# Kernel optimization log

Hardware: AMD Instinct MI355X
Metric: run time of the kernel (lower is better)

Reference implementation:

```python
import jax, jax.numpy as jnp
import numpy as np

T, B, I, H = 512, 64, 1024, 1024


def setup_inputs() -> dict:
    key = jax.random.key(0)
    ks = jax.random.split(key, 16)
    s_i = 1.0 / np.sqrt(I)  # mimic nn.Linear init scale
    s_h = 1.0 / np.sqrt(H)
    inp = {
        "x": jax.random.normal(ks[0], (T, B, I), dtype=jnp.float32),
        "hidden": jax.random.normal(ks[1], (B, H), dtype=jnp.float32),
        # update gate
        "Wzi": jax.random.normal(ks[2], (H, I), dtype=jnp.float32) * s_i,
        "bzi": jax.random.normal(ks[3], (H,), dtype=jnp.float32) * s_i,
        "Wzh": jax.random.normal(ks[4], (H, H), dtype=jnp.float32) * s_h,
        "bzh": jax.random.normal(ks[5], (H,), dtype=jnp.float32) * s_h,
        # reset gate
        "Wri": jax.random.normal(ks[6], (H, I), dtype=jnp.float32) * s_i,
        "bri": jax.random.normal(ks[7], (H,), dtype=jnp.float32) * s_i,
        "Wrh": jax.random.normal(ks[8], (H, H), dtype=jnp.float32) * s_h,
        "brh": jax.random.normal(ks[9], (H,), dtype=jnp.float32) * s_h,
        # candidate hidden
        "Wci": jax.random.normal(ks[10], (H, I), dtype=jnp.float32) * s_i,
        "bci": jax.random.normal(ks[11], (H,), dtype=jnp.float32) * s_i,
        "Wch": jax.random.normal(ks[12], (H, H), dtype=jnp.float32) * s_h,
        "bch": jax.random.normal(ks[13], (H,), dtype=jnp.float32) * s_h,
    }
    return inp


def reference(x, hidden, Wzi, bzi, Wzh, bzh, Wri, bri, Wrh, brh, Wci, bci, Wch, bch):
    # Pre-compute all input-to-hidden projections in one batched GEMM per gate:
    # [T,B,I] @ [I,H] -> [T,B,H]. Same math as per-step Linear calls.
    xz = jnp.einsum('tbi,hi->tbh', x, Wzi) + bzi
    xr = jnp.einsum('tbi,hi->tbh', x, Wri) + bri
    xc = jnp.einsum('tbi,hi->tbh', x, Wci) + bci

    def step(h, xt):
        xz_t, xr_t, xc_t = xt
        z = jax.nn.sigmoid(xz_t + h @ Wzh.T + bzh)
        r = jax.nn.sigmoid(xr_t + h @ Wrh.T + brh)
        candh = jnp.tanh(xc_t + (r * h) @ Wch.T + bch)
        h_new = (1.0 - z) * h + z * candh
        return h_new, h_new

    hidden_final, output = jax.lax.scan(step, hidden, (xz, xr, xc))
    return output, hidden_final


if __name__ == "__main__":
    out = reference(**setup_inputs())
    print(out[0].shape, out[1].shape)
```

## Files before the change

### kernel.cpp

```cpp
#include <hip/hip_runtime.h>


typedef __bf16 bf16x8 __attribute__((ext_vector_type(8)));
typedef float  f32x4  __attribute__((ext_vector_type(4)));

#define TT 512
#define BB 64
#define HH 1024

__global__ __launch_bounds__(256) void cvt_w(const float* __restrict__ src,
                                             __bf16* __restrict__ dst) {
    int i = (blockIdx.x * 256 + threadIdx.x) * 4;
    f32x4 v = *(const f32x4*)(src + i);
    __bf16 o[4] = {(__bf16)v.x, (__bf16)v.y, (__bf16)v.z, (__bf16)v.w};
    *(ulong1*)(dst + i) = *(ulong1*)o;
}

__global__ __launch_bounds__(256) void gru_init(const float* __restrict__ hid,
                                                float* __restrict__ h_f,
                                                __bf16* __restrict__ h_b) {
    int i = blockIdx.x * 256 + threadIdx.x;
    if (i < BB * HH) {
        float v = hid[i];
        h_f[i] = v;
        h_b[i] = (__bf16)v;
    }
}

__device__ __forceinline__ bf16x8 ld_cvt8(const float* p) {
    f32x4 a = *(const f32x4*)p;
    f32x4 b = *(const f32x4*)(p + 4);
    bf16x8 r;
    r[0] = (__bf16)a.x; r[1] = (__bf16)a.y; r[2] = (__bf16)a.z; r[3] = (__bf16)a.w;
    r[4] = (__bf16)b.x; r[5] = (__bf16)b.y; r[6] = (__bf16)b.z; r[7] = (__bf16)b.w;
    return r;
}

__global__ __launch_bounds__(64) void gru_zr(
    const float* __restrict__ x_t, const __bf16* __restrict__ h_b,
    const float* __restrict__ h_f,
    const __bf16* __restrict__ Wzh, const __bf16* __restrict__ Wzi,
    const float* __restrict__ bzh, const float* __restrict__ bzi,
    const __bf16* __restrict__ Wrh, const __bf16* __restrict__ Wri,
    const float* __restrict__ brh, const float* __restrict__ bri,
    float* __restrict__ zbuf, __bf16* __restrict__ rh)
{
    const int gate_r = blockIdx.x >> 8;
    const int tile   = blockIdx.x & 255;
    const int m0 = (tile & 3) << 4;
    const int n0 = (tile >> 2) << 4;
    const int lane = threadIdx.x;
    const int rc = lane & 15;
    const int kg = lane >> 4;

    const __bf16* Wh = gate_r ? Wrh : Wzh;
    const __bf16* Wi = gate_r ? Wri : Wzi;

    const __bf16* A1 = h_b + (m0 + rc) * HH + kg * 8;
    const __bf16* B1 = Wh  + (n0 + rc) * HH + kg * 8;
    const float*  A2 = x_t + (m0 + rc) * HH + kg * 8;
    const __bf16* B2 = Wi  + (n0 + rc) * HH + kg * 8;

    f32x4 acc = {0.f, 0.f, 0.f, 0.f};
    #pragma unroll 8
    for (int k = 0; k < HH; k += 32) {
        bf16x8 a = *(const bf16x8*)(A1 + k);
        bf16x8 b = *(const bf16x8*)(B1 + k);
        acc = __builtin_amdgcn_mfma_f32_16x16x32_bf16(a, b, acc, 0, 0, 0);
    }
    #pragma unroll 8
    for (int k = 0; k < HH; k += 32) {
        bf16x8 a = ld_cvt8(A2 + k);
        bf16x8 b = *(const bf16x8*)(B2 + k);
        acc = __builtin_amdgcn_mfma_f32_16x16x32_bf16(a, b, acc, 0, 0, 0);
    }

    const int n = n0 + rc;
    const float bias = gate_r ? (brh[n] + bri[n]) : (bzh[n] + bzi[n]);
    #pragma unroll
    for (int r = 0; r < 4; ++r) {
        const int m = m0 + kg * 4 + r;
        const int idx = m * HH + n;
        const float v = acc[r] + bias;
        const float s = 1.f / (1.f + __expf(-v));
        if (gate_r) rh[idx]   = (__bf16)(s * h_f[idx]);
        else        zbuf[idx] = s;
    }
}

__global__ __launch_bounds__(64) void gru_c(
    const float* __restrict__ x_t, const __bf16* __restrict__ rh,
    const __bf16* __restrict__ Wch, const __bf16* __restrict__ Wci,
    const float* __restrict__ bch, const float* __restrict__ bci,
    const float* __restrict__ zbuf,
    float* __restrict__ h_f, __bf16* __restrict__ h_b,
    float* __restrict__ out_t, float* __restrict__ out_tail, int last)
{
    const int tile = blockIdx.x;
    const int m0 = (tile & 3) << 4;
    const int n0 = (tile >> 2) << 4;
    const int lane = threadIdx.x;
    const int rc = lane & 15;
    const int kg = lane >> 4;

    const __bf16* A1 = rh  + (m0 + rc) * HH + kg * 8;
    const __bf16* B1 = Wch + (n0 + rc) * HH + kg * 8;
    const float*  A2 = x_t + (m0 + rc) * HH + kg * 8;
    const __bf16* B2 = Wci + (n0 + rc) * HH + kg * 8;

    f32x4 acc = {0.f, 0.f, 0.f, 0.f};
    #pragma unroll 8
    for (int k = 0; k < HH; k += 32) {
        bf16x8 a = *(const bf16x8*)(A1 + k);
        bf16x8 b = *(const bf16x8*)(B1 + k);
        acc = __builtin_amdgcn_mfma_f32_16x16x32_bf16(a, b, acc, 0, 0, 0);
    }
    #pragma unroll 8
    for (int k = 0; k < HH; k += 32) {
        bf16x8 a = ld_cvt8(A2 + k);
        bf16x8 b = *(const bf16x8*)(B2 + k);
        acc = __builtin_amdgcn_mfma_f32_16x16x32_bf16(a, b, acc, 0, 0, 0);
    }

    const int n = n0 + rc;
    const float bias = bch[n] + bci[n];
    #pragma unroll
    for (int r = 0; r < 4; ++r) {
        const int m = m0 + kg * 4 + r;
        const int idx = m * HH + n;
        const float c = tanhf(acc[r] + bias);
        const float z = zbuf[idx];
        const float hn = (1.f - z) * h_f[idx] + z * c;
        h_f[idx] = hn;
        h_b[idx] = (__bf16)hn;
        out_t[idx] = hn;
        if (last) out_tail[idx] = hn;
    }
}

extern "C" void kernel_launch(void* const* d_in, const int* in_sizes, int n_in,
                              void* d_out, int out_size, void* d_ws, size_t ws_size,
                              hipStream_t stream) {
    const float* x   = (const float*)d_in[0];
    const float* hid = (const float*)d_in[1];
    const float* Wzi = (const float*)d_in[2];
    const float* bzi = (const float*)d_in[3];
    const float* Wzh = (const float*)d_in[4];
    const float* bzh = (const float*)d_in[5];
    const float* Wri = (const float*)d_in[6];
    const float* bri = (const float*)d_in[7];
    const float* Wrh = (const float*)d_in[8];
    const float* brh = (const float*)d_in[9];
    const float* Wci = (const float*)d_in[10];
    const float* bci = (const float*)d_in[11];
    const float* Wch = (const float*)d_in[12];
    const float* bch = (const float*)d_in[13];
    float* out = (float*)d_out;

    char* ws = (char*)d_ws;
    const size_t WSZ = (size_t)HH * HH * sizeof(__bf16);
    __bf16* Wzh_b = (__bf16*)(ws + 0 * WSZ);
    __bf16* Wzi_b = (__bf16*)(ws + 1 * WSZ);
    __bf16* Wrh_b = (__bf16*)(ws + 2 * WSZ);
    __bf16* Wri_b = (__bf16*)(ws + 3 * WSZ);
    __bf16* Wch_b = (__bf16*)(ws + 4 * WSZ);
    __bf16* Wci_b = (__bf16*)(ws + 5 * WSZ);
    char* p = ws + 6 * WSZ;
    float*  zbuf = (float*)p;             p += (size_t)BB * HH * 4;
    float*  h_f  = (float*)p;             p += (size_t)BB * HH * 4;
    __bf16* h_b  = (__bf16*)p;            p += (size_t)BB * HH * 2;
    __bf16* rh   = (__bf16*)p;

    const int cvt_blocks = (HH * HH) / (256 * 4);
    cvt_w<<<cvt_blocks, 256, 0, stream>>>(Wzh, Wzh_b);
    cvt_w<<<cvt_blocks, 256, 0, stream>>>(Wzi, Wzi_b);
    cvt_w<<<cvt_blocks, 256, 0, stream>>>(Wrh, Wrh_b);
    cvt_w<<<cvt_blocks, 256, 0, stream>>>(Wri, Wri_b);
    cvt_w<<<cvt_blocks, 256, 0, stream>>>(Wch, Wch_b);
    cvt_w<<<cvt_blocks, 256, 0, stream>>>(Wci, Wci_b);
    gru_init<<<256, 256, 0, stream>>>(hid, h_f, h_b);

    for (int t = 0; t < TT; ++t) {
        const float* x_t = x + (size_t)t * BB * HH;
        gru_zr<<<512, 64, 0, stream>>>(x_t, h_b, h_f,
                                       Wzh_b, Wzi_b, bzh, bzi,
                                       Wrh_b, Wri_b, brh, bri,
                                       zbuf, rh);
        gru_c<<<256, 64, 0, stream>>>(x_t, rh, Wch_b, Wci_b, bch, bci,
                                      zbuf, h_f, h_b,
                                      out + (size_t)t * BB * HH,
                                      out + (size_t)TT * BB * HH,
                                      (t == TT - 1) ? 1 : 0);
    }
}
```

Baseline: 12.83 ms.

## Fuse GRU timesteps into one persistent kernel with grid-wide barriers

Replaces the 1024 per-step kernel launches with a single persistent kernel of 64 workgroups that loops over all timesteps and synchronises through atomic global barriers. Each workgroup owns a 16-column slice of the hidden units, keeps z in registers and the bf16 x_t tile in LDS, and splits the candidate GEMM's K dimension across wave pairs, combining the halves through LDS. The input projections for the next step are computed while waiting at the barrier, hiding them behind the recurrence. The cost is that only 64 CUs do the work, and progress depends on all workgroups being co-resident and on the spin barrier, which adds latency at each step.

```diff
diff --git a/kernel.cpp b/kernel.cpp
--- a/kernel.cpp
+++ b/kernel.cpp
@@ -4,9 +4,12 @@
 typedef __bf16 bf16x8 __attribute__((ext_vector_type(8)));
 typedef float  f32x4  __attribute__((ext_vector_type(4)));
 
-#define TT 512
-#define BB 64
-#define HH 1024
+#define TT  512
+#define BB  64
+#define HH  1024
+#define BHH (BB * HH)
+#define NWG 64
+#define NT  512
 
 __global__ __launch_bounds__(256) void cvt_w(const float* __restrict__ src,
                                              __bf16* __restrict__ dst) {
@@ -18,123 +21,176 @@
 
 __global__ __launch_bounds__(256) void gru_init(const float* __restrict__ hid,
                                                 float* __restrict__ h_f,
-                                                __bf16* __restrict__ h_b) {
+                                                __bf16* __restrict__ h_b,
+                                                unsigned* __restrict__ bar) {
     int i = blockIdx.x * 256 + threadIdx.x;
-    if (i < BB * HH) {
+    if (i < BHH) {
         float v = hid[i];
         h_f[i] = v;
         h_b[i] = (__bf16)v;
     }
-}
-
-__device__ __forceinline__ bf16x8 ld_cvt8(const float* p) {
-    f32x4 a = *(const f32x4*)p;
-    f32x4 b = *(const f32x4*)(p + 4);
-    bf16x8 r;
-    r[0] = (__bf16)a.x; r[1] = (__bf16)a.y; r[2] = (__bf16)a.z; r[3] = (__bf16)a.w;
-    r[4] = (__bf16)b.x; r[5] = (__bf16)b.y; r[6] = (__bf16)b.z; r[7] = (__bf16)b.w;
-    return r;
-}
-
-__global__ __launch_bounds__(64) void gru_zr(
-    const float* __restrict__ x_t, const __bf16* __restrict__ h_b,
-    const float* __restrict__ h_f,
+    if (i == 0) { bar[0] = 0u; bar[1] = 0u; }
+}
+
+template<int NK>
+__device__ __forceinline__ f32x4 mm_g(const __bf16* __restrict__ A,
+                                      const __bf16* __restrict__ B, f32x4 acc) {
+    #pragma unroll 8
+    for (int k = 0; k < NK; k += 32) {
+        bf16x8 a = *(const bf16x8*)(A + k);
+        bf16x8 b = *(const bf16x8*)(B + k);
+        acc = __builtin_amdgcn_mfma_f32_16x16x32_bf16(a, b, acc, 0, 0, 0);
+    }
+    return acc;
+}
+
+template<int NK>
+__device__ __forceinline__ f32x4 mm_x(const char* xl, unsigned rowb,
+                                      unsigned coff, unsigned rmask,
+                                      const __bf16* __restrict__ B, f32x4 acc) {
+    #pragma unroll 8
+    for (int k = 0; k < NK; k += 32) {
+        bf16x8 a = *(const bf16x8*)(xl + rowb + ((coff + (unsigned)(k * 2)) ^ rmask));
+        bf16x8 b = *(const bf16x8*)(B + k);
+        acc = __builtin_amdgcn_mfma_f32_16x16x32_bf16(a, b, acc, 0, 0, 0);
+    }
+    return acc;
+}
+
+__device__ __forceinline__ void stage_x(char* xl, const float* __restrict__ xt) {
+    const int tid = threadIdx.x;
+    #pragma unroll
+    for (int p = 0; p < 16; ++p) {
+        int c = p * NT + tid;
+        unsigned row = (unsigned)(c >> 7);
+        unsigned off = (unsigned)(c & 127) << 4;
+        const float* s = xt + ((size_t)c << 3);
+        f32x4 v0 = *(const f32x4*)s;
+        f32x4 v1 = *(const f32x4*)(s + 4);
+        bf16x8 ov;
+        ov[0] = (__bf16)v0.x; ov[1] = (__bf16)v0.y; ov[2] = (__bf16)v0.z; ov[3] = (__bf16)v0.w;
+        ov[4] = (__bf16)v1.x; ov[5] = (__bf16)v1.y; ov[6] = (__bf16)v1.z; ov[7] = (__bf16)v1.w;
+        *(bf16x8*)(xl + row * 2048u + (off ^ ((row & 7u) << 4))) = ov;
+    }
+}
+
+__device__ __forceinline__ void gbar_arrive(unsigned* bar, unsigned target) {
+    __syncthreads();
+    if (threadIdx.x == 0) {
+        __threadfence();
+        unsigned old = __hip_atomic_fetch_add(&bar[0], 1u, __ATOMIC_ACQ_REL,
+                                              __HIP_MEMORY_SCOPE_AGENT);
+        if (old == (unsigned)(NWG - 1)) {
+            __hip_atomic_store(&bar[0], 0u, __ATOMIC_RELAXED, __HIP_MEMORY_SCOPE_AGENT);
+            __hip_atomic_store(&bar[1], target, __ATOMIC_RELEASE, __HIP_MEMORY_SCOPE_AGENT);
+        }
+    }
+}
+
+__device__ __forceinline__ void gbar_wait(unsigned* bar, unsigned target) {
+    if (threadIdx.x == 0) {
+        while (__hip_atomic_load(&bar[1], __ATOMIC_ACQUIRE, __HIP_MEMORY_SCOPE_AGENT) < target)
+            __builtin_amdgcn_s_sleep(2);
+        __threadfence();
+    }
+    __syncthreads();
+}
+
+__global__ __launch_bounds__(NT) void gru_fused(
+    const float* __restrict__ x,
     const __bf16* __restrict__ Wzh, const __bf16* __restrict__ Wzi,
+    const __bf16* __restrict__ Wrh, const __bf16* __restrict__ Wri,
+    const __bf16* __restrict__ Wch, const __bf16* __restrict__ Wci,
     const float* __restrict__ bzh, const float* __restrict__ bzi,
-    const __bf16* __restrict__ Wrh, const __bf16* __restrict__ Wri,
     const float* __restrict__ brh, const float* __restrict__ bri,
-    float* __restrict__ zbuf, __bf16* __restrict__ rh)
+    const float* __restrict__ bch, const float* __restrict__ bci,
+    float* __restrict__ h_f, __bf16* __restrict__ h_b,
+    __bf16* __restrict__ rh, unsigned* __restrict__ bar,
+    float* __restrict__ out)
 {
-    const int gate_r = blockIdx.x >> 8;
-    const int tile   = blockIdx.x & 255;
-    const int m0 = (tile & 3) << 4;
-    const int n0 = (tile >> 2) << 4;
-    const int lane = threadIdx.x;
-    const int rc = lane & 15;
-    const int kg = lane >> 4;
-
-    const __bf16* Wh = gate_r ? Wrh : Wzh;
-    const __bf16* Wi = gate_r ? Wri : Wzi;
-
-    const __bf16* A1 = h_b + (m0 + rc) * HH + kg * 8;
-    const __bf16* B1 = Wh  + (n0 + rc) * HH + kg * 8;
-    const float*  A2 = x_t + (m0 + rc) * HH + kg * 8;
-    const __bf16* B2 = Wi  + (n0 + rc) * HH + kg * 8;
-
-    f32x4 acc = {0.f, 0.f, 0.f, 0.f};
-    #pragma unroll 8
-    for (int k = 0; k < HH; k += 32) {
-        bf16x8 a = *(const bf16x8*)(A1 + k);
-        bf16x8 b = *(const bf16x8*)(B1 + k);
-        acc = __builtin_amdgcn_mfma_f32_16x16x32_bf16(a, b, acc, 0, 0, 0);
-    }
-    #pragma unroll 8
-    for (int k = 0; k < HH; k += 32) {
-        bf16x8 a = ld_cvt8(A2 + k);
-        bf16x8 b = *(const bf16x8*)(B2 + k);
-        acc = __builtin_amdgcn_mfma_f32_16x16x32_bf16(a, b, acc, 0, 0, 0);
-    }
-
-    const int n = n0 + rc;
-    const float bias = gate_r ? (brh[n] + bri[n]) : (bzh[n] + bzi[n]);
-    #pragma unroll
-    for (int r = 0; r < 4; ++r) {
-        const int m = m0 + kg * 4 + r;
-        const int idx = m * HH + n;
-        const float v = acc[r] + bias;
-        const float s = 1.f / (1.f + __expf(-v));
-        if (gate_r) rh[idx]   = (__bf16)(s * h_f[idx]);
-        else        zbuf[idx] = s;
-    }
-}
-
-__global__ __launch_bounds__(64) void gru_c(
-    const float* __restrict__ x_t, const __bf16* __restrict__ rh,
-    const __bf16* __restrict__ Wch, const __bf16* __restrict__ Wci,
-    const float* __restrict__ bch, const float* __restrict__ bci,
-    const float* __restrict__ zbuf,
-    float* __restrict__ h_f, __bf16* __restrict__ h_b,
-    float* __restrict__ out_t, float* __restrict__ out_tail, int last)
-{
-    const int tile = blockIdx.x;
-    const int m0 = (tile & 3) << 4;
-    const int n0 = (tile >> 2) << 4;
-    const int lane = threadIdx.x;
-    const int rc = lane & 15;
-    const int kg = lane >> 4;
-
-    const __bf16* A1 = rh  + (m0 + rc) * HH + kg * 8;
-    const __bf16* B1 = Wch + (n0 + rc) * HH + kg * 8;
-    const float*  A2 = x_t + (m0 + rc) * HH + kg * 8;
-    const __bf16* B2 = Wci + (n0 + rc) * HH + kg * 8;
-
-    f32x4 acc = {0.f, 0.f, 0.f, 0.f};
-    #pragma unroll 8
-    for (int k = 0; k < HH; k += 32) {
-        bf16x8 a = *(const bf16x8*)(A1 + k);
-        bf16x8 b = *(const bf16x8*)(B1 + k);
-        acc = __builtin_amdgcn_mfma_f32_16x16x32_bf16(a, b, acc, 0, 0, 0);
-    }
-    #pragma unroll 8
-    for (int k = 0; k < HH; k += 32) {
-        bf16x8 a = ld_cvt8(A2 + k);
-        bf16x8 b = *(const bf16x8*)(B2 + k);
-        acc = __builtin_amdgcn_mfma_f32_16x16x32_bf16(a, b, acc, 0, 0, 0);
-    }
-
-    const int n = n0 + rc;
-    const float bias = bch[n] + bci[n];
-    #pragma unroll
-    for (int r = 0; r < 4; ++r) {
-        const int m = m0 + kg * 4 + r;
-        const int idx = m * HH + n;
-        const float c = tanhf(acc[r] + bias);
-        const float z = zbuf[idx];
-        const float hn = (1.f - z) * h_f[idx] + z * c;
-        h_f[idx] = hn;
-        h_b[idx] = (__bf16)hn;
-        out_t[idx] = hn;
-        if (last) out_tail[idx] = hn;
+    __shared__ __align__(16) char smem[132 * 1024];
+    char* xl = smem;
+    f32x4* red = (f32x4*)(smem + 131072);
+
+    const int wg   = blockIdx.x;
+    const int n0   = wg << 4;
+    const int tid  = threadIdx.x;
+    const int wv   = tid >> 6;
+    const int lane = tid & 63;
+    const int rc   = lane & 15;
+    const int kg   = lane >> 4;
+    const int mt   = wv >> 1;
+    const int odd  = wv & 1;
+    const int m0   = mt << 4;
+
+    const int n  = n0 + rc;
+    const float bz = bzh[n] + bzi[n];
+    const float br = brh[n] + bri[n];
+    const float bc = bch[n] + bci[n];
+
+    const int arow = (m0 + rc) * HH + kg * 8;
+    const int brow = n * HH + kg * 8;
+    const unsigned xrowb = (unsigned)(m0 + rc) * 2048u;
+    const unsigned xmask = ((unsigned)(m0 + rc) & 7u) << 4;
+    const unsigned xcoff = (unsigned)kg * 16u;
+
+    const __bf16* Wh  = odd ? Wrh : Wzh;
+    const __bf16* Wxi = odd ? Wri : Wzi;
+    const f32x4 zero = {0.f, 0.f, 0.f, 0.f};
+
+    stage_x(xl, x);
+    __syncthreads();
+    f32x4 px = mm_x<1024>(xl, xrowb, xcoff, xmask, Wxi + brow, zero);
+
+    f32x4 zreg = zero;
+    unsigned target = 0;
+
+    for (int t = 0; t < TT; ++t) {
+        f32x4 acc = mm_g<1024>(h_b + arow, Wh + brow, zero);
+        if (odd) {
+            #pragma unroll
+            for (int r2 = 0; r2 < 4; ++r2) {
+                int idx = (m0 + kg * 4 + r2) * HH + n;
+                float s = 1.f / (1.f + __expf(-(acc[r2] + px[r2] + br)));
+                rh[idx] = (__bf16)(s * h_f[idx]);
+            }
+        } else {
+            #pragma unroll
+            for (int r2 = 0; r2 < 4; ++r2)
+                zreg[r2] = 1.f / (1.f + __expf(-(acc[r2] + px[r2] + bz)));
+        }
+        target++;
+        gbar_arrive(bar, target);
+        f32x4 pacc = mm_x<512>(xl, xrowb, xcoff + (odd ? 1024u : 0u), xmask,
+                               Wci + brow + (odd ? 512 : 0), zero);
+        gbar_wait(bar, target);
+
+        pacc = mm_g<512>(rh + arow + (odd ? 512 : 0),
+                         Wch + brow + (odd ? 512 : 0), pacc);
+        if (odd) red[mt * 64 + lane] = pacc;
+        __syncthreads();
+        if (!odd) {
+            f32x4 other = red[mt * 64 + lane];
+            #pragma unroll
+            for (int r2 = 0; r2 < 4; ++r2) {
+                int idx = (m0 + kg * 4 + r2) * HH + n;
+                float c  = tanhf(pacc[r2] + other[r2] + bc);
+                float ho = h_f[idx];
+                float hn = (1.f - zreg[r2]) * ho + zreg[r2] * c;
+                h_f[idx] = hn;
+                h_b[idx] = (__bf16)hn;
+                out[(size_t)t * BHH + idx] = hn;
+                if (t == TT - 1) out[(size_t)TT * BHH + idx] = hn;
+            }
+        }
+        target++;
+        gbar_arrive(bar, target);
+        if (t + 1 < TT) {
+            stage_x(xl, x + (size_t)(t + 1) * BHH);
+            __syncthreads();
+            px = mm_x<1024>(xl, xrowb, xcoff, xmask, Wxi + brow, zero);
+        }
+        gbar_wait(bar, target);
     }
 }
 
@@ -166,10 +222,10 @@
     __bf16* Wch_b = (__bf16*)(ws + 4 * WSZ);
     __bf16* Wci_b = (__bf16*)(ws + 5 * WSZ);
     char* p = ws + 6 * WSZ;
-    float*  zbuf = (float*)p;             p += (size_t)BB * HH * 4;
-    float*  h_f  = (float*)p;             p += (size_t)BB * HH * 4;
-    __bf16* h_b  = (__bf16*)p;            p += (size_t)BB * HH * 2;
-    __bf16* rh   = (__bf16*)p;
+    float*    h_f = (float*)p;    p += (size_t)BHH * 4;
+    __bf16*   h_b = (__bf16*)p;   p += (size_t)BHH * 2;
+    __bf16*   rh  = (__bf16*)p;   p += (size_t)BHH * 2;
+    unsigned* bar = (unsigned*)p;
 
     const int cvt_blocks = (HH * HH) / (256 * 4);
     cvt_w<<<cvt_blocks, 256, 0, stream>>>(Wzh, Wzh_b);
@@ -178,18 +234,10 @@
     cvt_w<<<cvt_blocks, 256, 0, stream>>>(Wri, Wri_b);
     cvt_w<<<cvt_blocks, 256, 0, stream>>>(Wch, Wch_b);
     cvt_w<<<cvt_blocks, 256, 0, stream>>>(Wci, Wci_b);
-    gru_init<<<256, 256, 0, stream>>>(hid, h_f, h_b);
-
-    for (int t = 0; t < TT; ++t) {
-        const float* x_t = x + (size_t)t * BB * HH;
-        gru_zr<<<512, 64, 0, stream>>>(x_t, h_b, h_f,
-                                       Wzh_b, Wzi_b, bzh, bzi,
-                                       Wrh_b, Wri_b, brh, bri,
-                                       zbuf, rh);
-        gru_c<<<256, 64, 0, stream>>>(x_t, rh, Wch_b, Wci_b, bch, bci,
-                                      zbuf, h_f, h_b,
-                                      out + (size_t)t * BB * HH,
-                                      out + (size_t)TT * BB * HH,
-                                      (t == TT - 1) ? 1 : 0);
-    }
-}
+    gru_init<<<BHH / 256, 256, 0, stream>>>(hid, h_f, h_b, bar);
+
+    gru_fused<<<NWG, NT, 0, stream>>>(x,
+                                      Wzh_b, Wzi_b, Wrh_b, Wri_b, Wch_b, Wci_b,
+                                      bzh, bzi, brh, bri, bch, bci,
+                                      h_f, h_b, rh, bar, out);
+}
```

After: 22.53 ms. +75.6%, slower.
